# Kernel tuning notes

Hardware: AMD Instinct MI355X
Metric: run time of the kernel (lower is better)

Reference implementation:

```python
import jax, jax.numpy as jnp
from jax import lax
import numpy as np

PROB_SIZE = 512  # m = n = prob_size
QP_ITERS = 20    # fixed-iteration differentiable projected-gradient QP solve (CvxpyLayer surrogate)


def setup_inputs() -> dict:
    key = jax.random.key(0)
    ks = jax.random.split(key, 4)
    b, p, d = 16, PROB_SIZE, 128
    mk = lambda k: jax.random.normal(k, (b, p, d), dtype=jnp.float32) * 0.05
    return {
        "n_emb_cur": mk(ks[0]),
        "e_emb_cur": mk(ks[1]),
        "n_emb_nxt": mk(ks[2]),
        "e_emb_nxt": mk(ks[3]),
    }


def _pairwise_sqdist(a, b):
    # Kpp_x1 + Kpp_x2 - 2*Kpp_g from the torch code: ||a_i||^2 + ||b_j||^2 - 2 a_i.b_j
    g = jnp.einsum('bid,bjd->bij', a, b)            # (b, m, n) Gram
    da = jnp.sum(a * a, axis=-1)[:, :, None]        # diag(a a^T) broadcast over j
    db = jnp.sum(b * b, axis=-1)[:, None, :]        # diag(b b^T) broadcast over i
    return da + db - 2.0 * g


def _get_Q(n_emb_cur, e_emb_cur, n_emb_nxt, e_emb_nxt):
    Kp = _pairwise_sqdist(n_emb_cur, n_emb_nxt)     # (b, m, n) node kernel
    Kq = _pairwise_sqdist(e_emb_cur, e_emb_nxt)     # (b, m, n) edge kernel
    bsz, m, n = Kp.shape
    # torch: Kp.transpose(1,2).reshape(b,-1)  -> n-major flattening (x[j*m+i])
    q = 0.5 * (Kp + Kq).transpose(0, 2, 1).reshape(bsz, n * m)
    return q


def _qp_solve(q, m, n, iters=QP_ITERS):
    # Fixed-iteration projected gradient descent, differentiable and jit-able.
    bsz = q.shape[0]
    qm = q.reshape(bsz, n, m)
    X0 = jnp.full((bsz, n, m), 1.0 / m, dtype=q.dtype)  # feasible init
    lr = 0.5 / (jnp.sum(qm * qm, axis=(1, 2), keepdims=True) + 1e-8)

    def step(X, _):
        s = jnp.sum(qm * X, axis=(1, 2), keepdims=True)   # q.x
        X = X - lr * (2.0 * s * qm)                        # gradient of (q.x)^2
        X = jnp.clip(X, 0.0, 1.0)                          # box constraint
        X = X / (jnp.sum(X, axis=2, keepdims=True) + 1e-8) # equality: row sums = 1
        col = jnp.sum(X, axis=1, keepdims=True)
        X = X * jnp.minimum(1.0, 2.0 / (col + 1e-8))       # inequality: col sums <= 2
        return X, None

    X, _ = lax.scan(step, X0, None, length=iters)
    return X.reshape(bsz, n * m)


def reference(n_emb_cur, e_emb_cur, n_emb_nxt, e_emb_nxt):
    m = n = PROB_SIZE
    q = _get_Q(n_emb_cur, e_emb_cur, n_emb_nxt, e_emb_nxt)  # (b, m*n) cost vector
    x_star = _qp_solve(q, m, n)                              # (b, m*n)
    return x_star
```

## Files before the change

### kernel.cpp

```cpp
#include <hip/hip_runtime.h>

#define BATCH 16
#define NN 512
#define MM 512
#define DD 128
#define QP_ITERS 20
#define NBLK (BATCH * 16)
#define SLOT 1024

typedef __attribute__((ext_vector_type(8))) short bf16x8;
typedef __attribute__((ext_vector_type(4))) float f32x4;

#define LDR 56

__device__ __forceinline__ unsigned short bf16_rne(float f) {
    unsigned u = __float_as_uint(f);
    return (unsigned short)((u + 0x7FFFu + ((u >> 16) & 1u)) >> 16);
}

__device__ __forceinline__ void split4(float4 v, uint2& hi, uint2& lo) {
    unsigned short h0 = bf16_rne(v.x), h1 = bf16_rne(v.y),
                   h2 = bf16_rne(v.z), h3 = bf16_rne(v.w);
    hi.x = (unsigned)h0 | ((unsigned)h1 << 16);
    hi.y = (unsigned)h2 | ((unsigned)h3 << 16);
    unsigned short l0 = bf16_rne(v.x - __uint_as_float((unsigned)h0 << 16));
    unsigned short l1 = bf16_rne(v.y - __uint_as_float((unsigned)h1 << 16));
    unsigned short l2 = bf16_rne(v.z - __uint_as_float((unsigned)h2 << 16));
    unsigned short l3 = bf16_rne(v.w - __uint_as_float((unsigned)h3 << 16));
    lo.x = (unsigned)l0 | ((unsigned)l1 << 16);
    lo.y = (unsigned)l2 | ((unsigned)l3 << 16);
}

__device__ __forceinline__ float dot4(float4 v) {
    return v.x*v.x + v.y*v.y + v.z*v.z + v.w*v.w;
}

__global__ __launch_bounds__(256, 2) void gemm_q_kernel(
    const float* __restrict__ nc, const float* __restrict__ ec,
    const float* __restrict__ nn, const float* __restrict__ en,
    float* __restrict__ qm, float* __restrict__ qsums,
    float* __restrict__ q2sums, unsigned* __restrict__ flags)
{
    int b  = blockIdx.z;
    int it = blockIdx.x;
    int jt = blockIdx.y;
    int tid = threadIdx.x;

    if (it == 0 && jt == 0 && b == 0) {
        flags[tid] = 0u; flags[tid + 256] = 0u;
    }

    __shared__ __align__(16) unsigned short sAh[64 * LDR];
    __shared__ __align__(16) unsigned short sAl[64 * LDR];
    __shared__ __align__(16) unsigned short sBh[128 * LDR];
    __shared__ __align__(16) unsigned short sBl[128 * LDR];

    int l  = tid & 63;
    int wv = tid >> 6;
    int wi = wv & 1;
    int wj = wv >> 1;
    int lm = l & 15;
    int lg = l >> 4;

    int ar  = tid >> 2, akq = (tid & 3) * 8;
    int br  = tid >> 1, bk0 = (tid & 1) * 16;

    const float* aBase[2] = { nn + ((size_t)b*NN + jt*64)  * DD,
                              en + ((size_t)b*NN + jt*64)  * DD };
    const float* bBase[2] = { nc + ((size_t)b*MM + it*128) * DD,
                              ec + ((size_t)b*MM + it*128) * DD };

    f32x4 acc[2][4];
    #pragma unroll
    for (int a = 0; a < 2; ++a)
        #pragma unroll
        for (int c = 0; c < 4; ++c) acc[a][c] = (f32x4){0.f, 0.f, 0.f, 0.f};

    float s_a = 0.f, s_b = 0.f;

    for (int s = 0; s < 8; ++s) {
        const float* ga = aBase[s >> 2] + (size_t)ar * DD + (s & 3) * 32 + akq;
        const float* gb = bBase[s >> 2] + (size_t)br * DD + (s & 3) * 32 + bk0;
        float4 va0 = *(const float4*)(ga);
        float4 va1 = *(const float4*)(ga + 4);
        float4 vb0 = *(const float4*)(gb);
        float4 vb1 = *(const float4*)(gb + 4);
        float4 vb2 = *(const float4*)(gb + 8);
        float4 vb3 = *(const float4*)(gb + 12);
        s_a += dot4(va0) + dot4(va1);
        s_b += dot4(vb0) + dot4(vb1) + dot4(vb2) + dot4(vb3);

        __syncthreads();
        {
            uint2 h, lo;
            split4(va0, h, lo);
            *(uint2*)&sAh[ar*LDR + akq]     = h; *(uint2*)&sAl[ar*LDR + akq]     = lo;
            split4(va1, h, lo);
            *(uint2*)&sAh[ar*LDR + akq + 4] = h; *(uint2*)&sAl[ar*LDR + akq + 4] = lo;
            split4(vb0, h, lo);
            *(uint2*)&sBh[br*LDR + bk0]      = h; *(uint2*)&sBl[br*LDR + bk0]      = lo;
            split4(vb1, h, lo);
            *(uint2*)&sBh[br*LDR + bk0 + 4]  = h; *(uint2*)&sBl[br*LDR + bk0 + 4]  = lo;
            split4(vb2, h, lo);
            *(uint2*)&sBh[br*LDR + bk0 + 8]  = h; *(uint2*)&sBl[br*LDR + bk0 + 8]  = lo;
            split4(vb3, h, lo);
            *(uint2*)&sBh[br*LDR + bk0 + 12] = h; *(uint2*)&sBl[br*LDR + bk0 + 12] = lo;
        }
        __syncthreads();

        bf16x8 ah[2], al[2];
        #pragma unroll
        for (int jf = 0; jf < 2; ++jf) {
            int rr = wj*32 + jf*16 + lm;
            ah[jf] = *(const bf16x8*)&sAh[rr*LDR + lg*8];
            al[jf] = *(const bf16x8*)&sAl[rr*LDR + lg*8];
        }
        #pragma unroll
        for (int ff = 0; ff < 4; ++ff) {
            int rr = wi*64 + ff*16 + lm;
            bf16x8 bh = *(const bf16x8*)&sBh[rr*LDR + lg*8];
            bf16x8 bl = *(const bf16x8*)&sBl[rr*LDR + lg*8];
            #pragma unroll
            for (int jf = 0; jf < 2; ++jf) {
                acc[jf][ff] = __builtin_amdgcn_mfma_f32_16x16x32_bf16(
                                  ah[jf], bh, acc[jf][ff], 0, 0, 0);
                acc[jf][ff] = __builtin_amdgcn_mfma_f32_16x16x32_bf16(
                                  ah[jf], bl, acc[jf][ff], 0, 0, 0);
                acc[jf][ff] = __builtin_amdgcn_mfma_f32_16x16x32_bf16(
                                  al[jf], bh, acc[jf][ff], 0, 0, 0);
            }
        }
    }

    __syncthreads();
    float* nA = (float*)sAh;
    float* nB = nA + 256;
    nA[tid] = s_a;
    nB[tid] = s_b;
    __syncthreads();

    float rci[4];
    #pragma unroll
    for (int ff = 0; ff < 4; ++ff) {
        int i_loc = wi*64 + ff*16 + lm;
        rci[ff] = nB[2*i_loc] + nB[2*i_loc + 1];
    }

    float qs = 0.f, q2s = 0.f;
    #pragma unroll
    for (int jf = 0; jf < 2; ++jf) {
        #pragma unroll
        for (int r = 0; r < 4; ++r) {
            int j_loc = wj*32 + jf*16 + lg*4 + r;
            float rnj = nA[4*j_loc] + nA[4*j_loc+1]
                      + nA[4*j_loc+2] + nA[4*j_loc+3];
            size_t rowp = ((size_t)b*NN + jt*64 + j_loc) * MM + it*128;
            #pragma unroll
            for (int ff = 0; ff < 4; ++ff) {
                float v = 0.5f * (rci[ff] + rnj) - acc[jf][ff][r];
                qm[rowp + wi*64 + ff*16 + lm] = v;
                qs += v; q2s += v * v;
            }
        }
    }

    #pragma unroll
    for (int off = 32; off; off >>= 1) {
        qs  += __shfl_down(qs,  off);
        q2s += __shfl_down(q2s, off);
    }
    __shared__ float red[8];
    int lane = tid & 63;
    if (lane == 0) { red[wv] = qs; red[4 + wv] = q2s; }
    __syncthreads();
    if (tid == 0) {
        int tile = b * 32 + jt * 4 + it;
        qsums[tile]  = red[0] + red[1] + red[2] + red[3];
        q2sums[tile] = red[4] + red[5] + red[6] + red[7];
    }
}

__device__ __forceinline__ float gather16_sum_agent(const float* p)
{
    float acc = 0.f;
    #pragma unroll
    for (int g2 = 0; g2 < 16; ++g2)
        acc += __hip_atomic_load((float*)(p + g2 * SLOT), __ATOMIC_RELAXED,
                                 __HIP_MEMORY_SCOPE_AGENT);
    return acc;
}

__global__ __launch_bounds__(1024, 4) void qp_iter_kernel(
    const float* __restrict__ qm, const float* __restrict__ qsums,
    const float* __restrict__ q2sums, float* __restrict__ part,
    unsigned* __restrict__ flags, float* __restrict__ out)
{
    __shared__ float lds[16384 + 1024 + 16];
    __shared__ int sh_ok;
    float* stage = lds + 16384;
    float* wred  = lds + 16384 + 1024;

    int tid   = threadIdx.x;
    int blk   = blockIdx.x;
    int b     = blk >> 4;
    int g     = blk & 15;
    int w     = tid >> 6;
    int lane  = tid & 63;
    int r_loc = tid >> 5;
    int cseg  = tid & 31;
    int j     = g * 32 + r_loc;

    size_t rowbase = ((size_t)b * NN + j) * MM;

    if (w == 0) {
        float v1 = (lane < 32) ? qsums[b * 32 + lane]  : 0.f;
        float v2 = (lane < 32) ? q2sums[b * 32 + lane] : 0.f;
        #pragma unroll
        for (int m = 32; m; m >>= 1) {
            v1 += __shfl_xor(v1, m);
            v2 += __shfl_xor(v2, m);
        }
        if (lane == 0) { wred[0] = v1; wred[1] = v2; }
    }

    float q[16], x[16], fk[16];
    #pragma unroll
    for (int k = 0; k < 16; ++k) q[k] = qm[rowbase + cseg + 32*k];

    const float inv_m = 1.0f / (float)MM;
    #pragma unroll
    for (int k = 0; k < 16; ++k) { x[k] = inv_m; fk[k] = 1.0f; }

    __syncthreads();
    const float lr = 0.5f / (wred[1] + 1e-8f);
    float s = wred[0] * inv_m;

    unsigned* myflag = flags + b * 32 + g;
    unsigned* bflags = flags + b * 32;

    for (int t = 1; t <= QP_ITERS; ++t) {
        if (t > 1) {
            unsigned tt = (unsigned)(t - 1);
            if (w == 0) {
                unsigned v = (lane < 16)
                    ? __hip_atomic_load(bflags + lane, __ATOMIC_RELAXED,
                                        __HIP_MEMORY_SCOPE_AGENT)
                    : tt;
                int ok = __all(v >= tt);
                if (lane == 0) sh_ok = ok;
            }
            __syncthreads();

            const float* p = part + (size_t)((t - 1) & 1) * (NBLK * SLOT)
                           + (size_t)b * (16 * SLOT) + tid;
            float acc = gather16_sum_agent(p);

            if (!sh_ok) {
                if (w == 0) {
                    for (;;) {
                        unsigned v = (lane < 16)
                            ? __hip_atomic_load(bflags + lane, __ATOMIC_RELAXED,
                                                __HIP_MEMORY_SCOPE_AGENT)
                            : tt;
                        if (__all(v >= tt)) break;
                    }
                }
                __syncthreads();
                acc = gather16_sum_agent(p);
            }

            if (tid < 512) stage[tid] = fminf(1.0f, 2.0f / (acc + 1e-8f));
            else           stage[tid] = acc;
            __syncthreads();

            float v = 0.f;
            #pragma unroll
            for (int kk = 0; kk < 8; ++kk) {
                int c = lane + 64 * kk;
                v += stage[c] * stage[512 + c];
            }
            #pragma unroll
            for (int m = 32; m; m >>= 1) v += __shfl_xor(v, m);
            s = v;
            #pragma unroll
            for (int k = 0; k < 16; ++k) fk[k] = stage[cseg + 32*k];
        }

        float c = 2.0f * lr * s;
        float rp = 0.f;
        #pragma unroll
        for (int k = 0; k < 16; ++k) {
            float v = x[k] * fk[k] - c * q[k];
            v = fminf(fmaxf(v, 0.f), 1.f);
            x[k] = v;
            rp += v;
        }
        #pragma unroll
        for (int m = 16; m; m >>= 1) rp += __shfl_xor(rp, m);
        float inv = 1.0f / (rp + 1e-8f);
        #pragma unroll
        for (int k = 0; k < 16; ++k) x[k] *= inv;

        #pragma unroll
        for (int k = 0; k < 16; ++k) {
            float qx = q[k] * x[k];
            float px = x[k] + __shfl_xor(x[k], 32);
            float pq = qx   + __shfl_xor(qx,   32);
            int col = cseg + 32*k;
            if (lane < 32) lds[w * 512 + col]        = px;
            else           lds[8192 + w * 512 + col] = pq;
        }
        __syncthreads();
        {
            int arr = tid >> 9;
            int col = tid & 511;
            const float* basep = lds + arr * 8192 + col;
            float acc = 0.f;
            #pragma unroll
            for (int w2 = 0; w2 < 16; ++w2) acc += basep[w2 * 512];
            float* dst = part + (size_t)(t & 1) * (NBLK * SLOT)
                       + (size_t)blk * SLOT + tid;
            __hip_atomic_store(dst, acc, __ATOMIC_RELAXED,
                               __HIP_MEMORY_SCOPE_AGENT);
        }

        __syncthreads();
        if (tid == 0)
            __hip_atomic_store(myflag, (unsigned)t, __ATOMIC_RELEASE,
                               __HIP_MEMORY_SCOPE_AGENT);
    }

    {
        unsigned tt = (unsigned)QP_ITERS;
        if (w == 0) {
            for (;;) {
                unsigned v = (lane < 16)
                    ? __hip_atomic_load(bflags + lane, __ATOMIC_RELAXED,
                                        __HIP_MEMORY_SCOPE_AGENT)
                    : tt;
                if (__all(v >= tt)) break;
            }
        }
        __syncthreads();
        const float* p = part + (size_t)(QP_ITERS & 1) * (NBLK * SLOT)
                       + (size_t)b * (16 * SLOT) + tid;
        if (tid < 512) {
            float acc = gather16_sum_agent(p);
            stage[tid] = fminf(1.0f, 2.0f / (acc + 1e-8f));
        }
        __syncthreads();
        #pragma unroll
        for (int k = 0; k < 16; ++k)
            out[rowbase + cseg + 32*k] = x[k] * stage[cseg + 32*k];
    }
}

extern "C" void kernel_launch(void* const* d_in, const int* in_sizes, int n_in,
                              void* d_out, int out_size, void* d_ws, size_t ws_size,
                              hipStream_t stream)
{
    const float* nc = (const float*)d_in[0];
    const float* ec = (const float*)d_in[1];
    const float* nn = (const float*)d_in[2];
    const float* en = (const float*)d_in[3];
    float* out = (float*)d_out;

    float* ws = (float*)d_ws;
    const size_t QM_FLOATS = (size_t)BATCH * NN * MM;

    float* qm   = ws;
    float* part = ws + QM_FLOATS;
    float* qsums  = part + (size_t)2 * NBLK * SLOT;
    float* q2sums = qsums + 512;
    unsigned* flags = (unsigned*)(q2sums + 512);

    gemm_q_kernel<<<dim3(4, 8, BATCH), 256, 0, stream>>>(nc, ec, nn, en, qm,
                                                         qsums, q2sums, flags);

    qp_iter_kernel<<<dim3(NBLK), dim3(1024), 0, stream>>>(
        qm, qsums, q2sums, part, flags, out);
}
```

Baseline: 246.1 us.

## Fuse Q-matrix GEMM into persistent QP kernel, dropping global qm round-trip

Removes the separate GEMM kernel. Each persistent QP block now computes its own 32-row slice of the cost matrix with split-bf16 MFMAs, loading operands straight from global into registers, and stages the result in LDS instead of writing the full qm matrix to global and reading it back. Global sums are exchanged through a new flag/barrier phase, and flags are reset with a memset. This saves a kernel launch and about 16 MB of global traffic. In exchange, each block recomputes the norms of the full 512-row B side, the B operand loads bypass LDS sharing, and a 1024-thread block carries the GEMM phase with only a small output tile per wave.

```diff
diff --git a/kernel.cpp b/kernel.cpp
--- a/kernel.cpp
+++ b/kernel.cpp
@@ -7,11 +7,10 @@
 #define QP_ITERS 20
 #define NBLK (BATCH * 16)
 #define SLOT 1024
+#define QSTRIDE 524
 
 typedef __attribute__((ext_vector_type(8))) short bf16x8;
 typedef __attribute__((ext_vector_type(4))) float f32x4;
-
-#define LDR 56
 
 __device__ __forceinline__ unsigned short bf16_rne(float f) {
     unsigned u = __float_as_uint(f);
@@ -31,153 +30,20 @@
     lo.y = (unsigned)l2 | ((unsigned)l3 << 16);
 }
 
+union U8 { bf16x8 v; uint2 d[2]; };
+
+__device__ __forceinline__ void split8(float4 v0, float4 v1,
+                                       bf16x8& h8, bf16x8& l8) {
+    uint2 h0, l0, h1, l1;
+    split4(v0, h0, l0); split4(v1, h1, l1);
+    U8 th, tl;
+    th.d[0] = h0; th.d[1] = h1;
+    tl.d[0] = l0; tl.d[1] = l1;
+    h8 = th.v; l8 = tl.v;
+}
+
 __device__ __forceinline__ float dot4(float4 v) {
     return v.x*v.x + v.y*v.y + v.z*v.z + v.w*v.w;
-}
-
-__global__ __launch_bounds__(256, 2) void gemm_q_kernel(
-    const float* __restrict__ nc, const float* __restrict__ ec,
-    const float* __restrict__ nn, const float* __restrict__ en,
-    float* __restrict__ qm, float* __restrict__ qsums,
-    float* __restrict__ q2sums, unsigned* __restrict__ flags)
-{
-    int b  = blockIdx.z;
-    int it = blockIdx.x;
-    int jt = blockIdx.y;
-    int tid = threadIdx.x;
-
-    if (it == 0 && jt == 0 && b == 0) {
-        flags[tid] = 0u; flags[tid + 256] = 0u;
-    }
-
-    __shared__ __align__(16) unsigned short sAh[64 * LDR];
-    __shared__ __align__(16) unsigned short sAl[64 * LDR];
-    __shared__ __align__(16) unsigned short sBh[128 * LDR];
-    __shared__ __align__(16) unsigned short sBl[128 * LDR];
-
-    int l  = tid & 63;
-    int wv = tid >> 6;
-    int wi = wv & 1;
-    int wj = wv >> 1;
-    int lm = l & 15;
-    int lg = l >> 4;
-
-    int ar  = tid >> 2, akq = (tid & 3) * 8;
-    int br  = tid >> 1, bk0 = (tid & 1) * 16;
-
-    const float* aBase[2] = { nn + ((size_t)b*NN + jt*64)  * DD,
-                              en + ((size_t)b*NN + jt*64)  * DD };
-    const float* bBase[2] = { nc + ((size_t)b*MM + it*128) * DD,
-                              ec + ((size_t)b*MM + it*128) * DD };
-
-    f32x4 acc[2][4];
-    #pragma unroll
-    for (int a = 0; a < 2; ++a)
-        #pragma unroll
-        for (int c = 0; c < 4; ++c) acc[a][c] = (f32x4){0.f, 0.f, 0.f, 0.f};
-
-    float s_a = 0.f, s_b = 0.f;
-
-    for (int s = 0; s < 8; ++s) {
-        const float* ga = aBase[s >> 2] + (size_t)ar * DD + (s & 3) * 32 + akq;
-        const float* gb = bBase[s >> 2] + (size_t)br * DD + (s & 3) * 32 + bk0;
-        float4 va0 = *(const float4*)(ga);
-        float4 va1 = *(const float4*)(ga + 4);
-        float4 vb0 = *(const float4*)(gb);
-        float4 vb1 = *(const float4*)(gb + 4);
-        float4 vb2 = *(const float4*)(gb + 8);
-        float4 vb3 = *(const float4*)(gb + 12);
-        s_a += dot4(va0) + dot4(va1);
-        s_b += dot4(vb0) + dot4(vb1) + dot4(vb2) + dot4(vb3);
-
-        __syncthreads();
-        {
-            uint2 h, lo;
-            split4(va0, h, lo);
-            *(uint2*)&sAh[ar*LDR + akq]     = h; *(uint2*)&sAl[ar*LDR + akq]     = lo;
-            split4(va1, h, lo);
-            *(uint2*)&sAh[ar*LDR + akq + 4] = h; *(uint2*)&sAl[ar*LDR + akq + 4] = lo;
-            split4(vb0, h, lo);
-            *(uint2*)&sBh[br*LDR + bk0]      = h; *(uint2*)&sBl[br*LDR + bk0]      = lo;
-            split4(vb1, h, lo);
-            *(uint2*)&sBh[br*LDR + bk0 + 4]  = h; *(uint2*)&sBl[br*LDR + bk0 + 4]  = lo;
-            split4(vb2, h, lo);
-            *(uint2*)&sBh[br*LDR + bk0 + 8]  = h; *(uint2*)&sBl[br*LDR + bk0 + 8]  = lo;
-            split4(vb3, h, lo);
-            *(uint2*)&sBh[br*LDR + bk0 + 12] = h; *(uint2*)&sBl[br*LDR + bk0 + 12] = lo;
-        }
-        __syncthreads();
-
-        bf16x8 ah[2], al[2];
-        #pragma unroll
-        for (int jf = 0; jf < 2; ++jf) {
-            int rr = wj*32 + jf*16 + lm;
-            ah[jf] = *(const bf16x8*)&sAh[rr*LDR + lg*8];
-            al[jf] = *(const bf16x8*)&sAl[rr*LDR + lg*8];
-        }
-        #pragma unroll
-        for (int ff = 0; ff < 4; ++ff) {
-            int rr = wi*64 + ff*16 + lm;
-            bf16x8 bh = *(const bf16x8*)&sBh[rr*LDR + lg*8];
-            bf16x8 bl = *(const bf16x8*)&sBl[rr*LDR + lg*8];
-            #pragma unroll
-            for (int jf = 0; jf < 2; ++jf) {
-                acc[jf][ff] = __builtin_amdgcn_mfma_f32_16x16x32_bf16(
-                                  ah[jf], bh, acc[jf][ff], 0, 0, 0);
-                acc[jf][ff] = __builtin_amdgcn_mfma_f32_16x16x32_bf16(
-                                  ah[jf], bl, acc[jf][ff], 0, 0, 0);
-                acc[jf][ff] = __builtin_amdgcn_mfma_f32_16x16x32_bf16(
-                                  al[jf], bh, acc[jf][ff], 0, 0, 0);
-            }
-        }
-    }
-
-    __syncthreads();
-    float* nA = (float*)sAh;
-    float* nB = nA + 256;
-    nA[tid] = s_a;
-    nB[tid] = s_b;
-    __syncthreads();
-
-    float rci[4];
-    #pragma unroll
-    for (int ff = 0; ff < 4; ++ff) {
-        int i_loc = wi*64 + ff*16 + lm;
-        rci[ff] = nB[2*i_loc] + nB[2*i_loc + 1];
-    }
-
-    float qs = 0.f, q2s = 0.f;
-    #pragma unroll
-    for (int jf = 0; jf < 2; ++jf) {
-        #pragma unroll
-        for (int r = 0; r < 4; ++r) {
-            int j_loc = wj*32 + jf*16 + lg*4 + r;
-            float rnj = nA[4*j_loc] + nA[4*j_loc+1]
-                      + nA[4*j_loc+2] + nA[4*j_loc+3];
-            size_t rowp = ((size_t)b*NN + jt*64 + j_loc) * MM + it*128;
-            #pragma unroll
-            for (int ff = 0; ff < 4; ++ff) {
-                float v = 0.5f * (rci[ff] + rnj) - acc[jf][ff][r];
-                qm[rowp + wi*64 + ff*16 + lm] = v;
-                qs += v; q2s += v * v;
-            }
-        }
-    }
-
-    #pragma unroll
-    for (int off = 32; off; off >>= 1) {
-        qs  += __shfl_down(qs,  off);
-        q2s += __shfl_down(q2s, off);
-    }
-    __shared__ float red[8];
-    int lane = tid & 63;
-    if (lane == 0) { red[wv] = qs; red[4 + wv] = q2s; }
-    __syncthreads();
-    if (tid == 0) {
-        int tile = b * 32 + jt * 4 + it;
-        qsums[tile]  = red[0] + red[1] + red[2] + red[3];
-        q2sums[tile] = red[4] + red[5] + red[6] + red[7];
-    }
 }
 
 __device__ __forceinline__ float gather16_sum_agent(const float* p)
@@ -190,15 +56,20 @@
     return acc;
 }
 
-__global__ __launch_bounds__(1024, 4) void qp_iter_kernel(
-    const float* __restrict__ qm, const float* __restrict__ qsums,
-    const float* __restrict__ q2sums, float* __restrict__ part,
+__global__ __launch_bounds__(1024, 4) void qp_fused_kernel(
+    const float* __restrict__ nc, const float* __restrict__ ec,
+    const float* __restrict__ nn, const float* __restrict__ en,
+    float* __restrict__ part, float* __restrict__ sums_ex,
     unsigned* __restrict__ flags, float* __restrict__ out)
 {
-    __shared__ float lds[16384 + 1024 + 16];
+    __shared__ float lds[17424];
     __shared__ int sh_ok;
     float* stage = lds + 16384;
-    float* wred  = lds + 16384 + 1024;
+    float* wred  = lds + 17408;
+    float* qtile = lds;
+    float* rcs   = lds + 32*QSTRIDE;
+    float* rns   = lds + 32*QSTRIDE + 512;
+    float* redz  = lds + 32*QSTRIDE + 544;
 
     int tid   = threadIdx.x;
     int blk   = blockIdx.x;
@@ -209,12 +80,123 @@
     int r_loc = tid >> 5;
     int cseg  = tid & 31;
     int j     = g * 32 + r_loc;
-
     size_t rowbase = ((size_t)b * NN + j) * MM;
 
+    {
+        int lm = lane & 15, lg = lane >> 4;
+        const float* aB[2] = { nn + ((size_t)b*NN + g*32) * DD,
+                               en + ((size_t)b*NN + g*32) * DD };
+        const float* bB[2] = { nc + (size_t)b*MM*DD,
+                               ec + (size_t)b*MM*DD };
+
+        f32x4 acc[2][2];
+        #pragma unroll
+        for (int a = 0; a < 2; ++a)
+            #pragma unroll
+            for (int c = 0; c < 2; ++c) acc[a][c] = (f32x4){0.f,0.f,0.f,0.f};
+        float na[2] = {0.f, 0.f};
+        float nb[2] = {0.f, 0.f};
+
+        #pragma unroll
+        for (int s = 0; s < 8; ++s) {
+            const int mt = s >> 2;
+            const int kb = (s & 3) * 32 + lg * 8;
+            bf16x8 ah[2], al[2];
+            #pragma unroll
+            for (int jf = 0; jf < 2; ++jf) {
+                const float* ga = aB[mt] + (size_t)(jf*16 + lm)*DD + kb;
+                float4 v0 = *(const float4*)(ga);
+                float4 v1 = *(const float4*)(ga + 4);
+                na[jf] += dot4(v0) + dot4(v1);
+                split8(v0, v1, ah[jf], al[jf]);
+            }
+            #pragma unroll
+            for (int f = 0; f < 2; ++f) {
+                const float* gb = bB[mt] + (size_t)(w*32 + f*16 + lm)*DD + kb;
+                float4 v0 = *(const float4*)(gb);
+                float4 v1 = *(const float4*)(gb + 4);
+                nb[f] += dot4(v0) + dot4(v1);
+                bf16x8 bh, bl;
+                split8(v0, v1, bh, bl);
+                #pragma unroll
+                for (int jf = 0; jf < 2; ++jf) {
+                    acc[jf][f] = __builtin_amdgcn_mfma_f32_16x16x32_bf16(
+                                     ah[jf], bh, acc[jf][f], 0, 0, 0);
+                    acc[jf][f] = __builtin_amdgcn_mfma_f32_16x16x32_bf16(
+                                     ah[jf], bl, acc[jf][f], 0, 0, 0);
+                    acc[jf][f] = __builtin_amdgcn_mfma_f32_16x16x32_bf16(
+                                     al[jf], bh, acc[jf][f], 0, 0, 0);
+                }
+            }
+        }
+
+        #pragma unroll
+        for (int a = 0; a < 2; ++a) {
+            na[a] += __shfl_xor(na[a], 16); na[a] += __shfl_xor(na[a], 32);
+            nb[a] += __shfl_xor(nb[a], 16); nb[a] += __shfl_xor(nb[a], 32);
+        }
+        if (lane < 16) {
+            if (w == 0) { rns[lane] = na[0]; rns[16 + lane] = na[1]; }
+            rcs[w*32 + lane]      = nb[0];
+            rcs[w*32 + 16 + lane] = nb[1];
+        }
+        #pragma unroll
+        for (int jf = 0; jf < 2; ++jf)
+            #pragma unroll
+            for (int f = 0; f < 2; ++f)
+                #pragma unroll
+                for (int r = 0; r < 4; ++r)
+                    qtile[(jf*16 + lg*4 + r)*QSTRIDE + w*32 + f*16 + lm]
+                        = acc[jf][f][r];
+    }
+    __syncthreads();
+
+    float q[16];
+    float qs = 0.f, q2s = 0.f;
+    #pragma unroll
+    for (int k = 0; k < 16; ++k) {
+        float v = 0.5f*(rcs[cseg + 32*k] + rns[r_loc])
+                - qtile[r_loc*QSTRIDE + cseg + 32*k];
+        q[k] = v; qs += v; q2s += v*v;
+    }
+    #pragma unroll
+    for (int m = 32; m; m >>= 1) {
+        qs  += __shfl_xor(qs,  m);
+        q2s += __shfl_xor(q2s, m);
+    }
+    if (lane == 0) { redz[w] = qs; redz[16 + w] = q2s; }
+    __syncthreads();
+
+    unsigned* bflags = flags + b * 16;
+    unsigned* myflag = bflags + g;
+    if (tid == 0) {
+        float s1 = 0.f, s2 = 0.f;
+        #pragma unroll
+        for (int i = 0; i < 16; ++i) { s1 += redz[i]; s2 += redz[16 + i]; }
+        __hip_atomic_store(sums_ex + blk*2,     s1, __ATOMIC_RELAXED,
+                           __HIP_MEMORY_SCOPE_AGENT);
+        __hip_atomic_store(sums_ex + blk*2 + 1, s2, __ATOMIC_RELAXED,
+                           __HIP_MEMORY_SCOPE_AGENT);
+        __hip_atomic_store(myflag, 1u, __ATOMIC_RELEASE,
+                           __HIP_MEMORY_SCOPE_AGENT);
+    }
+
     if (w == 0) {
-        float v1 = (lane < 32) ? qsums[b * 32 + lane]  : 0.f;
-        float v2 = (lane < 32) ? q2sums[b * 32 + lane] : 0.f;
+        for (;;) {
+            unsigned v = (lane < 16)
+                ? __hip_atomic_load(bflags + lane, __ATOMIC_RELAXED,
+                                    __HIP_MEMORY_SCOPE_AGENT)
+                : 1u;
+            if (__all(v >= 1u)) break;
+        }
+        float v1 = 0.f, v2 = 0.f;
+        if (lane < 16) {
+            const float* sp = sums_ex + (size_t)(b*16 + lane) * 2;
+            v1 = __hip_atomic_load(sp,     __ATOMIC_RELAXED,
+                                   __HIP_MEMORY_SCOPE_AGENT);
+            v2 = __hip_atomic_load(sp + 1, __ATOMIC_RELAXED,
+                                   __HIP_MEMORY_SCOPE_AGENT);
+        }
         #pragma unroll
         for (int m = 32; m; m >>= 1) {
             v1 += __shfl_xor(v1, m);
@@ -222,25 +204,18 @@
         }
         if (lane == 0) { wred[0] = v1; wred[1] = v2; }
     }
-
-    float q[16], x[16], fk[16];
-    #pragma unroll
-    for (int k = 0; k < 16; ++k) q[k] = qm[rowbase + cseg + 32*k];
-
+    __syncthreads();
+    const float lr = 0.5f / (wred[1] + 1e-8f);
     const float inv_m = 1.0f / (float)MM;
+    float s = wred[0] * inv_m;
+
+    float x[16], fk[16];
     #pragma unroll
     for (int k = 0; k < 16; ++k) { x[k] = inv_m; fk[k] = 1.0f; }
 
-    __syncthreads();
-    const float lr = 0.5f / (wred[1] + 1e-8f);
-    float s = wred[0] * inv_m;
-
-    unsigned* myflag = flags + b * 32 + g;
-    unsigned* bflags = flags + b * 32;
-
     for (int t = 1; t <= QP_ITERS; ++t) {
         if (t > 1) {
-            unsigned tt = (unsigned)(t - 1);
+            unsigned tt = (unsigned)t;
             if (w == 0) {
                 unsigned v = (lane < 16)
                     ? __hip_atomic_load(bflags + lane, __ATOMIC_RELAXED,
@@ -326,12 +301,12 @@
 
         __syncthreads();
         if (tid == 0)
-            __hip_atomic_store(myflag, (unsigned)t, __ATOMIC_RELEASE,
+            __hip_atomic_store(myflag, (unsigned)(t + 1), __ATOMIC_RELEASE,
                                __HIP_MEMORY_SCOPE_AGENT);
     }
 
     {
-        unsigned tt = (unsigned)QP_ITERS;
+        unsigned tt = (unsigned)(QP_ITERS + 1);
         if (w == 0) {
             for (;;) {
                 unsigned v = (lane < 16)
@@ -366,17 +341,12 @@
     float* out = (float*)d_out;
 
     float* ws = (float*)d_ws;
-    const size_t QM_FLOATS = (size_t)BATCH * NN * MM;
-
-    float* qm   = ws;
-    float* part = ws + QM_FLOATS;
-    float* qsums  = part + (size_t)2 * NBLK * SLOT;
-    float* q2sums = qsums + 512;
-    unsigned* flags = (unsigned*)(q2sums + 512);
-
-    gemm_q_kernel<<<dim3(4, 8, BATCH), 256, 0, stream>>>(nc, ec, nn, en, qm,
-                                                         qsums, q2sums, flags);
-
-    qp_iter_kernel<<<dim3(NBLK), dim3(1024), 0, stream>>>(
-        qm, qsums, q2sums, part, flags, out);
-}
+    float* part    = ws;
+    float* sums_ex = part + (size_t)2 * NBLK * SLOT;
+    unsigned* flags = (unsigned*)(sums_ex + 512);
+
+    hipMemsetAsync(flags, 0, NBLK * sizeof(unsigned), stream);
+
+    qp_fused_kernel<<<dim3(NBLK), dim3(1024), 0, stream>>>(
+        nc, ec, nn, en, part, sums_ex, flags, out);
+}
```

New measurement: 349.0 us. +41.8%, slower.
